# Kernel optimization log

Measured on AMD Instinct MI355X. Metric: run time of the kernel, lower is better.

The kernel has to match this reference:

```python
import jax, jax.numpy as jnp
import numpy as np

R = 64          # plane_resolution
C = 32          # plane_channels
H = 128         # mlp_hidden
FEAT = 3 * C


def _grid_sample_bilinear(plane, coords):
    # plane: [C, R, R]; coords: [M, 2] normalized to [-1, 1], (x->W, y->H)
    # align_corners=True, padding_mode='border'
    r = plane.shape[-1]
    ix = (coords[:, 0] + 1.0) * 0.5 * (r - 1)
    iy = (coords[:, 1] + 1.0) * 0.5 * (r - 1)
    ix = jnp.clip(ix, 0.0, r - 1.0)
    iy = jnp.clip(iy, 0.0, r - 1.0)
    x0 = jnp.floor(ix).astype(jnp.int32)
    y0 = jnp.floor(iy).astype(jnp.int32)
    x1 = jnp.minimum(x0 + 1, r - 1)
    y1 = jnp.minimum(y0 + 1, r - 1)
    wx = ix - x0.astype(ix.dtype)
    wy = iy - y0.astype(iy.dtype)
    v00 = plane[:, y0, x0]  # [C, M]
    v01 = plane[:, y0, x1]
    v10 = plane[:, y1, x0]
    v11 = plane[:, y1, x1]
    out = (v00 * (1 - wx) * (1 - wy) + v01 * wx * (1 - wy)
           + v10 * (1 - wx) * wy + v11 * wx * wy)
    return out.T  # [M, C]


def setup_inputs() -> dict:
    key = jax.random.key(0)
    ks = jax.random.split(key, 12)
    B, N = 4, 262144
    points = jax.random.uniform(ks[0], (B, N, 3), dtype=jnp.float32)  # in [0,1) subset of [-1,1]
    planes = jax.random.normal(ks[1], (3, C, R, R), dtype=jnp.float32) * 0.01
    def lin(k, fan_in, fan_out):
        kw, kb = jax.random.split(k)
        bound = 1.0 / np.sqrt(fan_in)
        W = jax.random.uniform(kw, (fan_out, fan_in), jnp.float32, -bound, bound)
        b = jax.random.uniform(kb, (fan_out,), jnp.float32, -bound, bound)
        return W, b
    dW1, db1 = lin(ks[2], FEAT, H)
    dW2, db2 = lin(ks[3], H, H)
    dW3, db3 = lin(ks[4], H, 1)
    rW1, rb1 = lin(ks[5], FEAT, H)
    rW2, rb2 = lin(ks[6], H, 3)
    return dict(points=points, planes=planes,
                dW1=dW1, db1=db1, dW2=dW2, db2=db2, dW3=dW3, db3=db3,
                rW1=rW1, rb1=rb1, rW2=rW2, rb2=rb2)


def reference(points, planes, dW1, db1, dW2, db2, dW3, db3, rW1, rb1, rW2, rb2):
    B, N, _ = points.shape
    p = points.reshape(B * N, 3)
    x, y, z = p[:, 0], p[:, 1], p[:, 2]
    # coords for xy, xz, yz planes: [3, M, 2]
    coords = jnp.stack([jnp.stack([x, y], -1),
                        jnp.stack([x, z], -1),
                        jnp.stack([y, z], -1)], 0)
    feats = jax.vmap(_grid_sample_bilinear)(planes, coords)  # [3, M, C]
    feat = jnp.concatenate([feats[0], feats[1], feats[2]], axis=-1)  # [M, 3C]
    h = jax.nn.relu(feat @ dW1.T + db1)
    h = jax.nn.relu(h @ dW2.T + db2)
    density = jax.nn.softplus(h @ dW3.T + db3)  # [M, 1]
    r = jax.nn.relu(feat @ rW1.T + rb1)
    rgb = jax.nn.sigmoid(r @ rW2.T + rb2)  # [M, 3]
    return rgb.reshape(B, N, 3), density.reshape(B, N, 1)
```

## Files before the change

### kernel.cpp

```cpp
#include <hip/hip_runtime.h>
#include <hip/hip_bf16.h>
#include <math.h>

#define RR 64
#define CC 32
#define NPTS (4*262144)

typedef __attribute__((ext_vector_type(8))) short short8;
typedef __attribute__((ext_vector_type(4))) float f32x4;
typedef __attribute__((ext_vector_type(4))) unsigned int u32x4;

static __device__ inline ushort f2bf(float x) {
    return __builtin_bit_cast(ushort, __float2bfloat16(x));
}
static __device__ inline uint32_t pk2(float a, float b) {
    return (uint32_t)f2bf(a) | ((uint32_t)f2bf(b) << 16);
}
static __device__ inline float relu(float x) { return fmaxf(x, 0.0f); }


__global__ void prepass(const float* __restrict__ planes,
                        const float* __restrict__ dW1, const float* __restrict__ rW1,
                        const float* __restrict__ dW2,
                        const float* __restrict__ db1, const float* __restrict__ rb1,
                        const float* __restrict__ db2, const float* __restrict__ dW3,
                        const float* __restrict__ rW2,
                        float* __restrict__ ws) {
    int tid = blockIdx.x * blockDim.x + threadIdx.x;
    ushort* W1T = (ushort*)(ws + 393216);
    ushort* W2T = W1T + 24576;
    float*  CWS = ws + 393216 + 20480;

    if (tid < 3 * CC * RR * RR) {
        int x = tid % RR, y = (tid / RR) % RR, ch = (tid / (RR * RR)) % CC, p = tid / (CC * RR * RR);
        ws[((p * RR + y) * RR + x) * CC + ch] = planes[tid];
    }
    if (tid < 24576) {
        int e = tid & 7, l = (tid >> 3) & 63, rem = tid >> 9;
        int p = rem % 3, nt = rem / 3;
        int j = nt * 16 + (l & 15);
        int k = p * 32 + (l >> 4) * 8 + e;
        float v = (j < 128) ? dW1[j * 96 + k] : rW1[(j - 128) * 96 + k];
        W1T[tid] = f2bf(v);
    }
    if (tid < 16384) {
        int e = tid & 7, l = (tid >> 3) & 63, rem = tid >> 9;
        int kt2 = rem & 3, nt2 = rem >> 2;
        int j2 = nt2 * 16 + (l & 15);
        int k = kt2 * 32 + (l >> 4) * 8 + e;
        W2T[tid] = f2bf(dW2[j2 * 128 + k]);
    }
    if (tid < 256) CWS[tid]       = (tid < 128) ? db1[tid] : rb1[tid - 128];
    if (tid < 128) CWS[256 + tid] = db2[tid];
    if (tid < 128) CWS[384 + tid] = dW3[tid];
    if (tid < 384) CWS[512 + tid] = rW2[tid];
}

static __device__ inline short8 sample_frag(const float* __restrict__ P,
                                            int plane_base, float cx, float cy, int g8) {
    float ix = (cx + 1.0f) * 31.5f; ix = fminf(fmaxf(ix, 0.0f), 63.0f);
    float iy = (cy + 1.0f) * 31.5f; iy = fminf(fmaxf(iy, 0.0f), 63.0f);
    int x0 = (int)ix, y0 = (int)iy;
    int x1 = min(x0 + 1, 63), y1 = min(y0 + 1, 63);
    float wx = ix - (float)x0, wy = iy - (float)y0;
    float w00 = (1.0f - wx) * (1.0f - wy), w01 = wx * (1.0f - wy);
    float w10 = (1.0f - wx) * wy,          w11 = wx * wy;
    int b00 = plane_base + (y0 * 64 + x0) * 32 + g8;
    int b01 = plane_base + (y0 * 64 + x1) * 32 + g8;
    int b10 = plane_base + (y1 * 64 + x0) * 32 + g8;
    int b11 = plane_base + (y1 * 64 + x1) * 32 + g8;
    f32x4 a0 = *(const f32x4*)(P + b00), a1 = *(const f32x4*)(P + b00 + 4);
    f32x4 c0 = *(const f32x4*)(P + b01), c1 = *(const f32x4*)(P + b01 + 4);
    f32x4 d0 = *(const f32x4*)(P + b10), d1 = *(const f32x4*)(P + b10 + 4);
    f32x4 e0 = *(const f32x4*)(P + b11), e1 = *(const f32x4*)(P + b11 + 4);
    float f0 = w00 * a0[0] + w01 * c0[0] + w10 * d0[0] + w11 * e0[0];
    float f1 = w00 * a0[1] + w01 * c0[1] + w10 * d0[1] + w11 * e0[1];
    float f2 = w00 * a0[2] + w01 * c0[2] + w10 * d0[2] + w11 * e0[2];
    float f3 = w00 * a0[3] + w01 * c0[3] + w10 * d0[3] + w11 * e0[3];
    float f4 = w00 * a1[0] + w01 * c1[0] + w10 * d1[0] + w11 * e1[0];
    float f5 = w00 * a1[1] + w01 * c1[1] + w10 * d1[1] + w11 * e1[1];
    float f6 = w00 * a1[2] + w01 * c1[2] + w10 * d1[2] + w11 * e1[2];
    float f7 = w00 * a1[3] + w01 * c1[3] + w10 * d1[3] + w11 * e1[3];
    u32x4 uu;
    uu[0] = pk2(f0, f1); uu[1] = pk2(f2, f3);
    uu[2] = pk2(f4, f5); uu[3] = pk2(f6, f7);
    return __builtin_bit_cast(short8, uu);
}

#define MFMA(a, b, c) __builtin_amdgcn_mfma_f32_16x16x32_bf16((a), (b), (c), 0, 0, 0)

__global__ __launch_bounds__(1024, 1)
void nerf_mfma(const float* __restrict__ points, const float* __restrict__ ws,
               const float* __restrict__ db3g, const float* __restrict__ rb2g,
               float* __restrict__ rgb_out, float* __restrict__ den_out) {
    __shared__ __align__(16) ushort SB[42752];
    __shared__ __align__(16) ushort Hs[16][16][136];

    const float* P = ws;
    int tid = threadIdx.x;

    {
        const u32x4* src = (const u32x4*)(ws + 393216);
        u32x4* dst = (u32x4*)SB;
        for (int j = tid; j < 5344; j += 1024) dst[j] = src[j];
    }
    __syncthreads();

    const ushort* W1L = SB;
    const ushort* W2L = SB + 24576;
    const float*  Cl  = (const float*)(SB + 40960);

    int wid = tid >> 6, lane = tid & 63;
    int c = lane & 15, g = lane >> 4;
    int g8 = 8 * g;
    ushort (*H)[136] = Hs[wid];
    int gw = blockIdx.x * 16 + wid;

    float b3  = db3g[0];
    float rb0 = rb2g[0], rb1v = rb2g[1], rb2v = rb2g[2];

    for (int it = 0; it < 4; ++it) {
        int pbase = (gw * 4 + it) * 16;

        int ptA = pbase + c;
        float xa = points[ptA * 3 + 0], ya = points[ptA * 3 + 1], za = points[ptA * 3 + 2];
        short8 bfA0 = sample_frag(P, 0,      xa, ya, g8);
        short8 bfA1 = sample_frag(P, 131072, xa, za, g8);
        short8 bfA2 = sample_frag(P, 262144, ya, za, g8);

        #pragma unroll 4
        for (int nt = 0; nt < 8; ++nt) {
            const ushort* wp = W1L + nt * 1536 + lane * 8;
            short8 a0 = *(const short8*)(wp);
            short8 a1 = *(const short8*)(wp + 512);
            short8 a2 = *(const short8*)(wp + 1024);
            f32x4 accA = {0.f,0.f,0.f,0.f};
            accA = MFMA(a0, bfA0, accA);
            accA = MFMA(a1, bfA1, accA);
            accA = MFMA(a2, bfA2, accA);
            f32x4 bb = *(const f32x4*)(Cl + nt * 16 + 4 * g);
            uint2 wA;
            wA.x = pk2(relu(accA[0] + bb[0]), relu(accA[1] + bb[1]));
            wA.y = pk2(relu(accA[2] + bb[2]), relu(accA[3] + bb[3]));
            *(uint2*)(&H[c][16 * nt + 4 * g]) = wA;
        }

        float racc0A = 0.f, racc1A = 0.f, racc2A = 0.f;
        #pragma unroll 4
        for (int nt = 8; nt < 16; ++nt) {
            const ushort* wp = W1L + nt * 1536 + lane * 8;
            short8 a0 = *(const short8*)(wp);
            short8 a1 = *(const short8*)(wp + 512);
            short8 a2 = *(const short8*)(wp + 1024);
            f32x4 accA = {0.f,0.f,0.f,0.f};
            accA = MFMA(a0, bfA0, accA);
            accA = MFMA(a1, bfA1, accA);
            accA = MFMA(a2, bfA2, accA);
            int jo = (nt - 8) * 16 + 4 * g;
            f32x4 bb = *(const f32x4*)(Cl + 128 + jo);
            f32x4 w0 = *(const f32x4*)(Cl + 512 + jo);
            f32x4 w1 = *(const f32x4*)(Cl + 640 + jo);
            f32x4 w2 = *(const f32x4*)(Cl + 768 + jo);
            #pragma unroll
            for (int r = 0; r < 4; ++r) {
                float vA = relu(accA[r] + bb[r]);
                racc0A = fmaf(w0[r], vA, racc0A);
                racc1A = fmaf(w1[r], vA, racc1A);
                racc2A = fmaf(w2[r], vA, racc2A);
            }
        }

        asm volatile("s_waitcnt lgkmcnt(0)" ::: "memory");
        __builtin_amdgcn_sched_barrier(0);

        short8 b2A0 = *(const short8*)(&H[c][g8]);
        short8 b2A1 = *(const short8*)(&H[c][32 + g8]);
        short8 b2A2 = *(const short8*)(&H[c][64 + g8]);
        short8 b2A3 = *(const short8*)(&H[c][96 + g8]);

        float daccA = 0.f;
        #pragma unroll 2
        for (int nt2 = 0; nt2 < 8; ++nt2) {
            const ushort* wp = W2L + nt2 * 2048 + lane * 8;
            short8 a0 = *(const short8*)(wp);
            short8 a1 = *(const short8*)(wp + 512);
            short8 a2 = *(const short8*)(wp + 1024);
            short8 a3 = *(const short8*)(wp + 1536);
            f32x4 accA = {0.f,0.f,0.f,0.f};
            accA = MFMA(a0, b2A0, accA);
            accA = MFMA(a1, b2A1, accA);
            accA = MFMA(a2, b2A2, accA);
            accA = MFMA(a3, b2A3, accA);
            f32x4 bb = *(const f32x4*)(Cl + 256 + nt2 * 16 + 4 * g);
            f32x4 w3 = *(const f32x4*)(Cl + 384 + nt2 * 16 + 4 * g);
            #pragma unroll
            for (int r = 0; r < 4; ++r)
                daccA = fmaf(w3[r], relu(accA[r] + bb[r]), daccA);
        }

        {
            float v = daccA; v += __shfl_xor(v, 16, 64); v += __shfl_xor(v, 32, 64); v += b3;
            float sp = fmaxf(v, 0.0f) + log1pf(expf(-fabsf(v)));
            if (g == 0) den_out[ptA] = sp;
        }
        {
            float v = racc0A; v += __shfl_xor(v, 16, 64); v += __shfl_xor(v, 32, 64); v += rb0;
            if (g == 0) rgb_out[ptA * 3 + 0] = 1.0f / (1.0f + expf(-v));
        }
        {
            float v = racc1A; v += __shfl_xor(v, 16, 64); v += __shfl_xor(v, 32, 64); v += rb1v;
            if (g == 0) rgb_out[ptA * 3 + 1] = 1.0f / (1.0f + expf(-v));
        }
        {
            float v = racc2A; v += __shfl_xor(v, 16, 64); v += __shfl_xor(v, 32, 64); v += rb2v;
            if (g == 0) rgb_out[ptA * 3 + 2] = 1.0f / (1.0f + expf(-v));
        }

        asm volatile("" ::: "memory");
    }
}

extern "C" void kernel_launch(void* const* d_in, const int* in_sizes, int n_in,
                              void* d_out, int out_size, void* d_ws, size_t ws_size,
                              hipStream_t stream) {
    const float* points = (const float*)d_in[0];
    const float* planes = (const float*)d_in[1];
    const float* dW1    = (const float*)d_in[2];
    const float* db1    = (const float*)d_in[3];
    const float* dW2    = (const float*)d_in[4];
    const float* db2    = (const float*)d_in[5];
    const float* dW3    = (const float*)d_in[6];
    const float* db3    = (const float*)d_in[7];
    const float* rW1    = (const float*)d_in[8];
    const float* rb1    = (const float*)d_in[9];
    const float* rW2    = (const float*)d_in[10];
    const float* rb2    = (const float*)d_in[11];

    float* out     = (float*)d_out;
    float* rgb_out = out;
    float* den_out = out + 3 * NPTS;
    float* ws      = (float*)d_ws;

    prepass<<<1536, 256, 0, stream>>>(planes, dW1, rW1, dW2, db1, rb1,
                                      db2, dW3, rW2, ws);
    nerf_mfma<<<1024, 1024, 0, stream>>>(points, ws, db3, rb2, rgb_out, den_out);
}
```

Baseline: 224.0 us.

## Switch to 32x32x16 MFMA and pass hidden layer through registers instead of LDS

Replaces the 16x16x32 bf16 MFMA tiles with 32x32x16 tiles, processing 32 points per wave iteration and re-laying out the prepacked W1/W2 weights to match. The first hidden layer's output is repacked to bf16 and exchanged between lane halves with shuffles, so it can feed the second MFMA layer directly and the per-wave LDS staging buffer and its waitcnt barrier are removed. Epilogue math is vectorized with f32x4 ops. This adds register pressure from 16-wide accumulators and six sampled fragments per point group, and more shuffle traffic.

```diff
diff --git a/kernel.cpp b/kernel.cpp
--- a/kernel.cpp
+++ b/kernel.cpp
@@ -8,6 +8,7 @@
 
 typedef __attribute__((ext_vector_type(8))) short short8;
 typedef __attribute__((ext_vector_type(4))) float f32x4;
+typedef __attribute__((ext_vector_type(16))) float f32x16;
 typedef __attribute__((ext_vector_type(4))) unsigned int u32x4;
 
 static __device__ inline ushort f2bf(float x) {
@@ -16,7 +17,13 @@
 static __device__ inline uint32_t pk2(float a, float b) {
     return (uint32_t)f2bf(a) | ((uint32_t)f2bf(b) << 16);
 }
-static __device__ inline float relu(float x) { return fmaxf(x, 0.0f); }
+static __device__ inline f32x4 relu4(f32x4 v) {
+    f32x4 z = {0.f, 0.f, 0.f, 0.f};
+    return __builtin_elementwise_max(v, z);
+}
+static __device__ inline float hsum4(f32x4 v) {
+    return (v[0] + v[1]) + (v[2] + v[3]);
+}
 
 
 __global__ void prepass(const float* __restrict__ planes,
@@ -37,17 +44,17 @@
     }
     if (tid < 24576) {
         int e = tid & 7, l = (tid >> 3) & 63, rem = tid >> 9;
-        int p = rem % 3, nt = rem / 3;
-        int j = nt * 16 + (l & 15);
-        int k = p * 32 + (l >> 4) * 8 + e;
+        int kk = rem % 6, jt = rem / 6;
+        int j = jt * 32 + (l & 31);
+        int k = kk * 16 + (l >> 5) * 8 + e;
         float v = (j < 128) ? dW1[j * 96 + k] : rW1[(j - 128) * 96 + k];
         W1T[tid] = f2bf(v);
     }
     if (tid < 16384) {
         int e = tid & 7, l = (tid >> 3) & 63, rem = tid >> 9;
-        int kt2 = rem & 3, nt2 = rem >> 2;
-        int j2 = nt2 * 16 + (l & 15);
-        int k = kt2 * 32 + (l >> 4) * 8 + e;
+        int kk = rem & 7, jt2 = rem >> 3;
+        int j2 = jt2 * 32 + (l & 31);
+        int k = kk * 16 + (l >> 5) * 8 + e;
         W2T[tid] = f2bf(dW2[j2 * 128 + k]);
     }
     if (tid < 256) CWS[tid]       = (tid < 128) ? db1[tid] : rb1[tid - 128];
@@ -57,7 +64,7 @@
 }
 
 static __device__ inline short8 sample_frag(const float* __restrict__ P,
-                                            int plane_base, float cx, float cy, int g8) {
+                                            int plane_base, float cx, float cy, int chbase) {
     float ix = (cx + 1.0f) * 31.5f; ix = fminf(fmaxf(ix, 0.0f), 63.0f);
     float iy = (cy + 1.0f) * 31.5f; iy = fminf(fmaxf(iy, 0.0f), 63.0f);
     int x0 = (int)ix, y0 = (int)iy;
@@ -65,36 +72,64 @@
     float wx = ix - (float)x0, wy = iy - (float)y0;
     float w00 = (1.0f - wx) * (1.0f - wy), w01 = wx * (1.0f - wy);
     float w10 = (1.0f - wx) * wy,          w11 = wx * wy;
-    int b00 = plane_base + (y0 * 64 + x0) * 32 + g8;
-    int b01 = plane_base + (y0 * 64 + x1) * 32 + g8;
-    int b10 = plane_base + (y1 * 64 + x0) * 32 + g8;
-    int b11 = plane_base + (y1 * 64 + x1) * 32 + g8;
+    int b00 = plane_base + (y0 * 64 + x0) * 32 + chbase;
+    int b01 = plane_base + (y0 * 64 + x1) * 32 + chbase;
+    int b10 = plane_base + (y1 * 64 + x0) * 32 + chbase;
+    int b11 = plane_base + (y1 * 64 + x1) * 32 + chbase;
     f32x4 a0 = *(const f32x4*)(P + b00), a1 = *(const f32x4*)(P + b00 + 4);
     f32x4 c0 = *(const f32x4*)(P + b01), c1 = *(const f32x4*)(P + b01 + 4);
     f32x4 d0 = *(const f32x4*)(P + b10), d1 = *(const f32x4*)(P + b10 + 4);
     f32x4 e0 = *(const f32x4*)(P + b11), e1 = *(const f32x4*)(P + b11 + 4);
-    float f0 = w00 * a0[0] + w01 * c0[0] + w10 * d0[0] + w11 * e0[0];
-    float f1 = w00 * a0[1] + w01 * c0[1] + w10 * d0[1] + w11 * e0[1];
-    float f2 = w00 * a0[2] + w01 * c0[2] + w10 * d0[2] + w11 * e0[2];
-    float f3 = w00 * a0[3] + w01 * c0[3] + w10 * d0[3] + w11 * e0[3];
-    float f4 = w00 * a1[0] + w01 * c1[0] + w10 * d1[0] + w11 * e1[0];
-    float f5 = w00 * a1[1] + w01 * c1[1] + w10 * d1[1] + w11 * e1[1];
-    float f6 = w00 * a1[2] + w01 * c1[2] + w10 * d1[2] + w11 * e1[2];
-    float f7 = w00 * a1[3] + w01 * c1[3] + w10 * d1[3] + w11 * e1[3];
+    f32x4 flo = a0 * w00 + c0 * w01 + d0 * w10 + e0 * w11;
+    f32x4 fhi = a1 * w00 + c1 * w01 + d1 * w10 + e1 * w11;
     u32x4 uu;
-    uu[0] = pk2(f0, f1); uu[1] = pk2(f2, f3);
-    uu[2] = pk2(f4, f5); uu[3] = pk2(f6, f7);
+    uu[0] = pk2(flo[0], flo[1]); uu[1] = pk2(flo[2], flo[3]);
+    uu[2] = pk2(fhi[0], fhi[1]); uu[3] = pk2(fhi[2], fhi[3]);
     return __builtin_bit_cast(short8, uu);
 }
 
-#define MFMA(a, b, c) __builtin_amdgcn_mfma_f32_16x16x32_bf16((a), (b), (c), 0, 0, 0)
+#define MFMA32(a, b, c) __builtin_amdgcn_mfma_f32_32x32x16_bf16((a), (b), (c), 0, 0, 0)
+#define ZACC {0.f,0.f,0.f,0.f,0.f,0.f,0.f,0.f,0.f,0.f,0.f,0.f,0.f,0.f,0.f,0.f}
+
+#define DJT(jt, BLO, BHI) { \
+    const ushort* wa_ = W1L + (jt) * 3072 + lane * 8; \
+    f32x16 acc_ = ZACC; \
+    acc_ = MFMA32(*(const short8*)(wa_),        bf0, acc_); \
+    acc_ = MFMA32(*(const short8*)(wa_ + 512),  bf1, acc_); \
+    acc_ = MFMA32(*(const short8*)(wa_ + 1024), bf2, acc_); \
+    acc_ = MFMA32(*(const short8*)(wa_ + 1536), bf3, acc_); \
+    acc_ = MFMA32(*(const short8*)(wa_ + 2048), bf4, acc_); \
+    acc_ = MFMA32(*(const short8*)(wa_ + 2560), bf5, acc_); \
+    int jb_ = 32 * (jt) + h4; \
+    f32x4 av0_ = {acc_[0],  acc_[1],  acc_[2],  acc_[3]}; \
+    f32x4 av1_ = {acc_[4],  acc_[5],  acc_[6],  acc_[7]}; \
+    f32x4 av2_ = {acc_[8],  acc_[9],  acc_[10], acc_[11]}; \
+    f32x4 av3_ = {acc_[12], acc_[13], acc_[14], acc_[15]}; \
+    f32x4 v0_ = relu4(av0_ + *(const f32x4*)(Cl + jb_)); \
+    f32x4 v1_ = relu4(av1_ + *(const f32x4*)(Cl + jb_ + 8)); \
+    f32x4 v2_ = relu4(av2_ + *(const f32x4*)(Cl + jb_ + 16)); \
+    f32x4 v3_ = relu4(av3_ + *(const f32x4*)(Cl + jb_ + 24)); \
+    unsigned m0_ = pk2(v0_[0], v0_[1]), m1_ = pk2(v0_[2], v0_[3]); \
+    unsigned m2_ = pk2(v1_[0], v1_[1]), m3_ = pk2(v1_[2], v1_[3]); \
+    unsigned m4_ = pk2(v2_[0], v2_[1]), m5_ = pk2(v2_[2], v2_[3]); \
+    unsigned m6_ = pk2(v3_[0], v3_[1]), m7_ = pk2(v3_[2], v3_[3]); \
+    unsigned r0_ = __shfl_xor(m0_, 32, 64), r1_ = __shfl_xor(m1_, 32, 64); \
+    unsigned r2_ = __shfl_xor(m2_, 32, 64), r3_ = __shfl_xor(m3_, 32, 64); \
+    unsigned r4_ = __shfl_xor(m4_, 32, 64), r5_ = __shfl_xor(m5_, 32, 64); \
+    unsigned r6_ = __shfl_xor(m6_, 32, 64), r7_ = __shfl_xor(m7_, 32, 64); \
+    u32x4 lo_, hi_; \
+    lo_[0] = h ? r2_ : m0_;  lo_[1] = h ? r3_ : m1_; \
+    lo_[2] = h ? m2_ : r0_;  lo_[3] = h ? m3_ : r1_; \
+    hi_[0] = h ? r6_ : m4_;  hi_[1] = h ? r7_ : m5_; \
+    hi_[2] = h ? m6_ : r4_;  hi_[3] = h ? m7_ : r5_; \
+    BLO = __builtin_bit_cast(short8, lo_); \
+    BHI = __builtin_bit_cast(short8, hi_); }
 
 __global__ __launch_bounds__(1024, 1)
 void nerf_mfma(const float* __restrict__ points, const float* __restrict__ ws,
                const float* __restrict__ db3g, const float* __restrict__ rb2g,
                float* __restrict__ rgb_out, float* __restrict__ den_out) {
     __shared__ __align__(16) ushort SB[42752];
-    __shared__ __align__(16) ushort Hs[16][16][136];
 
     const float* P = ws;
     int tid = threadIdx.x;
@@ -111,112 +146,94 @@
     const float*  Cl  = (const float*)(SB + 40960);
 
     int wid = tid >> 6, lane = tid & 63;
-    int c = lane & 15, g = lane >> 4;
-    int g8 = 8 * g;
-    ushort (*H)[136] = Hs[wid];
+    int p5 = lane & 31;
+    int h  = lane >> 5;
+    int h8 = 8 * h, h4 = 4 * h;
     int gw = blockIdx.x * 16 + wid;
 
     float b3  = db3g[0];
     float rb0 = rb2g[0], rb1v = rb2g[1], rb2v = rb2g[2];
 
-    for (int it = 0; it < 4; ++it) {
-        int pbase = (gw * 4 + it) * 16;
-
-        int ptA = pbase + c;
-        float xa = points[ptA * 3 + 0], ya = points[ptA * 3 + 1], za = points[ptA * 3 + 2];
-        short8 bfA0 = sample_frag(P, 0,      xa, ya, g8);
-        short8 bfA1 = sample_frag(P, 131072, xa, za, g8);
-        short8 bfA2 = sample_frag(P, 262144, ya, za, g8);
-
-        #pragma unroll 4
-        for (int nt = 0; nt < 8; ++nt) {
-            const ushort* wp = W1L + nt * 1536 + lane * 8;
-            short8 a0 = *(const short8*)(wp);
-            short8 a1 = *(const short8*)(wp + 512);
-            short8 a2 = *(const short8*)(wp + 1024);
-            f32x4 accA = {0.f,0.f,0.f,0.f};
-            accA = MFMA(a0, bfA0, accA);
-            accA = MFMA(a1, bfA1, accA);
-            accA = MFMA(a2, bfA2, accA);
-            f32x4 bb = *(const f32x4*)(Cl + nt * 16 + 4 * g);
-            uint2 wA;
-            wA.x = pk2(relu(accA[0] + bb[0]), relu(accA[1] + bb[1]));
-            wA.y = pk2(relu(accA[2] + bb[2]), relu(accA[3] + bb[3]));
-            *(uint2*)(&H[c][16 * nt + 4 * g]) = wA;
-        }
-
-        float racc0A = 0.f, racc1A = 0.f, racc2A = 0.f;
-        #pragma unroll 4
-        for (int nt = 8; nt < 16; ++nt) {
-            const ushort* wp = W1L + nt * 1536 + lane * 8;
-            short8 a0 = *(const short8*)(wp);
-            short8 a1 = *(const short8*)(wp + 512);
-            short8 a2 = *(const short8*)(wp + 1024);
-            f32x4 accA = {0.f,0.f,0.f,0.f};
-            accA = MFMA(a0, bfA0, accA);
-            accA = MFMA(a1, bfA1, accA);
-            accA = MFMA(a2, bfA2, accA);
-            int jo = (nt - 8) * 16 + 4 * g;
-            f32x4 bb = *(const f32x4*)(Cl + 128 + jo);
-            f32x4 w0 = *(const f32x4*)(Cl + 512 + jo);
-            f32x4 w1 = *(const f32x4*)(Cl + 640 + jo);
-            f32x4 w2 = *(const f32x4*)(Cl + 768 + jo);
+    #pragma unroll
+    for (int it = 0; it < 2; ++it) {
+        int pt = (gw * 2 + it) * 32 + p5;
+        float x = points[pt * 3 + 0], y = points[pt * 3 + 1], z = points[pt * 3 + 2];
+
+        short8 bf0 = sample_frag(P, 0,      x, y, h8);
+        short8 bf1 = sample_frag(P, 0,      x, y, 16 + h8);
+        short8 bf2 = sample_frag(P, 131072, x, z, h8);
+        short8 bf3 = sample_frag(P, 131072, x, z, 16 + h8);
+        short8 bf4 = sample_frag(P, 262144, y, z, h8);
+        short8 bf5 = sample_frag(P, 262144, y, z, 16 + h8);
+
+        f32x4 rc0 = {0.f,0.f,0.f,0.f}, rc1 = {0.f,0.f,0.f,0.f}, rc2 = {0.f,0.f,0.f,0.f};
+        #pragma unroll
+        for (int jt = 4; jt < 8; ++jt) {
+            const ushort* wa = W1L + jt * 3072 + lane * 8;
+            f32x16 acc = ZACC;
+            acc = MFMA32(*(const short8*)(wa),        bf0, acc);
+            acc = MFMA32(*(const short8*)(wa + 512),  bf1, acc);
+            acc = MFMA32(*(const short8*)(wa + 1024), bf2, acc);
+            acc = MFMA32(*(const short8*)(wa + 1536), bf3, acc);
+            acc = MFMA32(*(const short8*)(wa + 2048), bf4, acc);
+            acc = MFMA32(*(const short8*)(wa + 2560), bf5, acc);
+            int jb = 32 * jt + h4;
+            int jo = 32 * (jt - 4) + h4;
             #pragma unroll
-            for (int r = 0; r < 4; ++r) {
-                float vA = relu(accA[r] + bb[r]);
-                racc0A = fmaf(w0[r], vA, racc0A);
-                racc1A = fmaf(w1[r], vA, racc1A);
-                racc2A = fmaf(w2[r], vA, racc2A);
+            for (int q = 0; q < 4; ++q) {
+                f32x4 av = {acc[4*q+0], acc[4*q+1], acc[4*q+2], acc[4*q+3]};
+                f32x4 bb = *(const f32x4*)(Cl + jb + 8 * q);
+                f32x4 v  = relu4(av + bb);
+                f32x4 w0 = *(const f32x4*)(Cl + 512 + jo + 8 * q);
+                f32x4 w1 = *(const f32x4*)(Cl + 640 + jo + 8 * q);
+                f32x4 w2 = *(const f32x4*)(Cl + 768 + jo + 8 * q);
+                rc0 += w0 * v; rc1 += w1 * v; rc2 += w2 * v;
             }
         }
-
-        asm volatile("s_waitcnt lgkmcnt(0)" ::: "memory");
-        __builtin_amdgcn_sched_barrier(0);
-
-        short8 b2A0 = *(const short8*)(&H[c][g8]);
-        short8 b2A1 = *(const short8*)(&H[c][32 + g8]);
-        short8 b2A2 = *(const short8*)(&H[c][64 + g8]);
-        short8 b2A3 = *(const short8*)(&H[c][96 + g8]);
-
-        float daccA = 0.f;
-        #pragma unroll 2
-        for (int nt2 = 0; nt2 < 8; ++nt2) {
-            const ushort* wp = W2L + nt2 * 2048 + lane * 8;
-            short8 a0 = *(const short8*)(wp);
-            short8 a1 = *(const short8*)(wp + 512);
-            short8 a2 = *(const short8*)(wp + 1024);
-            short8 a3 = *(const short8*)(wp + 1536);
-            f32x4 accA = {0.f,0.f,0.f,0.f};
-            accA = MFMA(a0, b2A0, accA);
-            accA = MFMA(a1, b2A1, accA);
-            accA = MFMA(a2, b2A2, accA);
-            accA = MFMA(a3, b2A3, accA);
-            f32x4 bb = *(const f32x4*)(Cl + 256 + nt2 * 16 + 4 * g);
-            f32x4 w3 = *(const f32x4*)(Cl + 384 + nt2 * 16 + 4 * g);
+        {
+            float v0 = hsum4(rc0), v1 = hsum4(rc1), v2 = hsum4(rc2);
+            v0 += __shfl_xor(v0, 32, 64);
+            v1 += __shfl_xor(v1, 32, 64);
+            v2 += __shfl_xor(v2, 32, 64);
+            if (h == 0) {
+                rgb_out[pt * 3 + 0] = 1.0f / (1.0f + expf(-(v0 + rb0)));
+                rgb_out[pt * 3 + 1] = 1.0f / (1.0f + expf(-(v1 + rb1v)));
+                rgb_out[pt * 3 + 2] = 1.0f / (1.0f + expf(-(v2 + rb2v)));
+            }
+        }
+
+        short8 c0, c1, c2, c3, c4, c5, c6, c7;
+        DJT(0, c0, c1) DJT(1, c2, c3) DJT(2, c4, c5) DJT(3, c6, c7)
+
+        f32x4 d4 = {0.f,0.f,0.f,0.f};
+        #pragma unroll
+        for (int jt2 = 0; jt2 < 4; ++jt2) {
+            const ushort* wa = W2L + jt2 * 4096 + lane * 8;
+            f32x16 acc = ZACC;
+            acc = MFMA32(*(const short8*)(wa),        c0, acc);
+            acc = MFMA32(*(const short8*)(wa + 512),  c1, acc);
+            acc = MFMA32(*(const short8*)(wa + 1024), c2, acc);
+            acc = MFMA32(*(const short8*)(wa + 1536), c3, acc);
+            acc = MFMA32(*(const short8*)(wa + 2048), c4, acc);
+            acc = MFMA32(*(const short8*)(wa + 2560), c5, acc);
+            acc = MFMA32(*(const short8*)(wa + 3072), c6, acc);
+            acc = MFMA32(*(const short8*)(wa + 3584), c7, acc);
+            int jb = 32 * jt2 + h4;
             #pragma unroll
-            for (int r = 0; r < 4; ++r)
-                daccA = fmaf(w3[r], relu(accA[r] + bb[r]), daccA);
-        }
-
+            for (int q = 0; q < 4; ++q) {
+                f32x4 av = {acc[4*q+0], acc[4*q+1], acc[4*q+2], acc[4*q+3]};
+                f32x4 bb = *(const f32x4*)(Cl + 256 + jb + 8 * q);
+                f32x4 w3 = *(const f32x4*)(Cl + 384 + jb + 8 * q);
+                d4 += w3 * relu4(av + bb);
+            }
+        }
         {
-            float v = daccA; v += __shfl_xor(v, 16, 64); v += __shfl_xor(v, 32, 64); v += b3;
-            float sp = fmaxf(v, 0.0f) + log1pf(expf(-fabsf(v)));
-            if (g == 0) den_out[ptA] = sp;
-        }
-        {
-            float v = racc0A; v += __shfl_xor(v, 16, 64); v += __shfl_xor(v, 32, 64); v += rb0;
-            if (g == 0) rgb_out[ptA * 3 + 0] = 1.0f / (1.0f + expf(-v));
-        }
-        {
-            float v = racc1A; v += __shfl_xor(v, 16, 64); v += __shfl_xor(v, 32, 64); v += rb1v;
-            if (g == 0) rgb_out[ptA * 3 + 1] = 1.0f / (1.0f + expf(-v));
-        }
-        {
-            float v = racc2A; v += __shfl_xor(v, 16, 64); v += __shfl_xor(v, 32, 64); v += rb2v;
-            if (g == 0) rgb_out[ptA * 3 + 2] = 1.0f / (1.0f + expf(-v));
-        }
-
-        asm volatile("" ::: "memory");
+            float dv = hsum4(d4);
+            dv += __shfl_xor(dv, 32, 64);
+            dv += b3;
+            float sp = fmaxf(dv, 0.0f) + log1pf(expf(-fabsf(dv)));
+            if (h == 0) den_out[pt] = sp;
+        }
     }
 }
 
```

After: 421.1 us. 1.88x slower.
